# Kernel optimization log

Measured on AMD Instinct MI355X. Metric: run time of the kernel, lower is better.

The kernel has to match this reference:

```python
import jax, jax.numpy as jnp
import numpy as np

H = 4      # num_heads (== num_v_heads)
DK = 128   # head_k_dim
DV = 256   # head_v_dim = head_dim * expand_v
NH = 2     # num_householder
HID = 1024 # hidden_size
KSZ = 4    # conv_size
EPS = 1e-5 # norm_eps


def short_conv(x, w):
    """Causal depthwise conv1d + SiLU. x: [B,T,C], w: [C,K]."""
    K = w.shape[1]
    T = x.shape[1]
    xp = jnp.pad(x, ((0, 0), (K - 1, 0), (0, 0)))
    y = sum(xp[:, i:i + T, :] * w[:, i] for i in range(K))
    return jax.nn.silu(y)


def l2norm(x, eps=1e-6):
    return x * jax.lax.rsqrt(jnp.sum(x * x, axis=-1, keepdims=True) + eps)


def setup_inputs() -> dict:
    key = jax.random.key(0)
    ks = jax.random.split(key, 16)
    s = 0.02
    B, T = 2, 1024
    return {
        "hidden_states": jax.random.normal(ks[0], (B, T, HID), jnp.float32),
        "Wq": jax.random.normal(ks[1], (HID, H * DK), jnp.float32) * s,
        "Wk": jax.random.normal(ks[2], (HID, NH * H * DK), jnp.float32) * s,
        "Wv": jax.random.normal(ks[3], (HID, NH * H * DV), jnp.float32) * s,
        "Wb": jax.random.normal(ks[4], (HID, NH * H), jnp.float32) * s,
        "Wa": jax.random.normal(ks[5], (HID, H), jnp.float32) * s,
        "Wg": jax.random.normal(ks[6], (HID, H * DV), jnp.float32) * s,
        "Wo": jax.random.normal(ks[7], (H * DV, HID), jnp.float32) * s,
        "A_log": jnp.log(jax.random.uniform(ks[8], (H,), jnp.float32, 0.5, 8.0)),
        "dt_bias": jax.random.normal(ks[9], (H,), jnp.float32) * 0.1,
        "wq_conv": jax.random.normal(ks[10], (H * DK, KSZ), jnp.float32) * 0.2,
        "wk_conv": jax.random.normal(ks[11], (NH * H * DK, KSZ), jnp.float32) * 0.2,
        "wv_conv": jax.random.normal(ks[12], (NH * H * DV, KSZ), jnp.float32) * 0.2,
        "o_norm_weight": jnp.ones((DV,), jnp.float32),
    }


def reference(hidden_states, Wq, Wk, Wv, Wb, Wa, Wg, Wo, A_log, dt_bias,
              wq_conv, wk_conv, wv_conv, o_norm_weight):
    B, T, _ = hidden_states.shape
    # projections + short conv (+ SiLU)
    q = short_conv(hidden_states @ Wq, wq_conv).reshape(B, T, H, DK)
    k = short_conv(hidden_states @ Wk, wk_conv).reshape(B, T, NH, H, DK)
    v = short_conv(hidden_states @ Wv, wv_conv).reshape(B, T, NH, H, DV)
    q = l2norm(q)
    k = l2norm(k)
    # beta: sigmoid * 2 (allow_neg_eigval), layout '(n h)'
    beta = 2.0 * jax.nn.sigmoid(hidden_states @ Wb).reshape(B, T, NH, H)
    # forget gate per token/head
    g = -jnp.exp(A_log) * jax.nn.softplus(hidden_states @ Wa + dt_bias)  # [B,T,H]

    def step(S, x):
        # S: [B,H,DK,DV]
        q_t, k_t, v_t, b_t, g_t = x
        S = S * jnp.exp(g_t)[..., None, None]  # token-level decay
        for i in range(NH):  # sequential Householder delta updates
            ki, vi, bi = k_t[:, i], v_t[:, i], b_t[:, i]
            kv = jnp.einsum('bhk,bhkv->bhv', ki, S)
            S = S + bi[..., None, None] * jnp.einsum('bhk,bhv->bhkv', ki, vi - kv)
        o_t = jnp.einsum('bhk,bhkv->bhv', q_t, S)
        return S, o_t

    xs = (q.transpose(1, 0, 2, 3), k.transpose(1, 0, 2, 3, 4),
          v.transpose(1, 0, 2, 3, 4), beta.transpose(1, 0, 2, 3),
          g.transpose(1, 0, 2))
    S0 = jnp.zeros((B, H, DK, DV), hidden_states.dtype)
    _, o = jax.lax.scan(jax.checkpoint(step), S0, xs)
    o = o.transpose(1, 0, 2, 3)  # [B,T,H,DV]

    # gated RMSNorm (FusedRMSNormGated): rmsnorm(o)*w * silu(gate)
    gate = (hidden_states @ Wg).reshape(B, T, H, DV)
    o = o * jax.lax.rsqrt(jnp.mean(o * o, axis=-1, keepdims=True) + EPS) * o_norm_weight
    o = o * jax.nn.silu(gate)
    return o.reshape(B, T, H * DV) @ Wo
```

## Files before the change

### kernel.cpp

```cpp
#include <hip/hip_runtime.h>
#include <cstdint>
#include <cstddef>

#define H 4
#define DK 128
#define DV 256
#define NH 2
#define HID 1024
#define KSZ 4
#define NTOT 4608

typedef __bf16 bfx8 __attribute__((ext_vector_type(8)));
typedef float f32x4 __attribute__((ext_vector_type(4)));

__device__ __forceinline__ float wave_sum(float x) {
#pragma unroll
  for (int off = 1; off < 64; off <<= 1) x += __shfl_xor(x, off, 64);
  return x;
}

__device__ __forceinline__ ushort f2bf(float x) {
  uint u = __float_as_uint(x);
  return (ushort)((u + 0x7fffu + ((u >> 16) & 1u)) >> 16);
}

#define DPP_ADD(x, ctrl) \
  x += __int_as_float(__builtin_amdgcn_update_dpp(0, __float_as_int(x), ctrl, 0xf, 0xf, true))

template <int N>
__device__ __forceinline__ void dpp_reduce(float (&d)[N]) {
#pragma unroll
  for (int i = 0; i < N; i++) DPP_ADD(d[i], 0x111);
#pragma unroll
  for (int i = 0; i < N; i++) DPP_ADD(d[i], 0x112);
#pragma unroll
  for (int i = 0; i < N; i++) DPP_ADD(d[i], 0x114);
#pragma unroll
  for (int i = 0; i < N; i++) DPP_ADD(d[i], 0x118);
#pragma unroll
  for (int i = 0; i < N; i++) DPP_ADD(d[i], 0x142);
#pragma unroll
  for (int i = 0; i < N; i++) DPP_ADD(d[i], 0x143);
#pragma unroll
  for (int i = 0; i < N; i++)
    d[i] = __int_as_float(__builtin_amdgcn_readlane(__float_as_int(d[i]), 63));
}

__global__ __launch_bounds__(256) void cast_hs(const float* __restrict__ src,
                                               ushort* __restrict__ dst) {
  int i = blockIdx.x * 256 + threadIdx.x;
  float4 v = ((const float4*)src)[i];
  ushort4 o = {f2bf(v.x), f2bf(v.y), f2bf(v.z), f2bf(v.w)};
  ((ushort4*)dst)[i] = o;
}

__global__ __launch_bounds__(256) void tr_pack(const float* __restrict__ Wq,
                                               const float* __restrict__ Wk,
                                               const float* __restrict__ Wv,
                                               const float* __restrict__ Wg,
                                               ushort* __restrict__ Bt) {
  __shared__ float tile[32][33];
  int n0 = blockIdx.x * 32, k0 = blockIdx.y * 32;
  const float* src;
  int ld, nb;
  if (n0 < 512)       { src = Wq; ld = 512;  nb = n0; }
  else if (n0 < 1536) { src = Wk; ld = 1024; nb = n0 - 512; }
  else if (n0 < 3584) { src = Wv; ld = 2048; nb = n0 - 1536; }
  else                { src = Wg; ld = 1024; nb = n0 - 3584; }
  int tx = threadIdx.x & 31, ty = threadIdx.x >> 5;
#pragma unroll
  for (int i = 0; i < 4; i++)
    tile[ty + i * 8][tx] = src[(size_t)(k0 + ty + i * 8) * ld + nb + tx];
  __syncthreads();
#pragma unroll
  for (int i = 0; i < 4; i++)
    Bt[(size_t)(n0 + ty + i * 8) * 1024 + k0 + tx] = f2bf(tile[tx][ty + i * 8]);
}

__global__ __launch_bounds__(256) void tr_one(const float* __restrict__ W,
                                              ushort* __restrict__ Bt, int N) {
  __shared__ float tile[32][33];
  int n0 = blockIdx.x * 32, k0 = blockIdx.y * 32;
  int tx = threadIdx.x & 31, ty = threadIdx.x >> 5;
#pragma unroll
  for (int i = 0; i < 4; i++)
    tile[ty + i * 8][tx] = W[(size_t)(k0 + ty + i * 8) * N + n0 + tx];
  __syncthreads();
#pragma unroll
  for (int i = 0; i < 4; i++)
    Bt[(size_t)(n0 + ty + i * 8) * 1024 + k0 + tx] = f2bf(tile[tx][ty + i * 8]);
}

#define LDP 40
__global__ __launch_bounds__(256) void gemm_bf16(const ushort* __restrict__ A,
                                                 const ushort* __restrict__ Bt,
                                                 float* __restrict__ C,
                                                 int K, int ldc) {
  __shared__ __align__(16) ushort As[128][LDP];
  __shared__ __align__(16) ushort Bs[128][LDP];
  const int tid = threadIdx.x;
  const int lane = tid & 63, wave = tid >> 6;
  const int wr = wave >> 1, wc = wave & 1;
  const int row0 = blockIdx.y * 128, col0 = blockIdx.x * 128;
  const int r = tid >> 1, hf = tid & 1;

  f32x4 acc[4][4];
#pragma unroll
  for (int i = 0; i < 4; i++)
#pragma unroll
    for (int j = 0; j < 4; j++) acc[i][j] = {0.f, 0.f, 0.f, 0.f};

  const int lrow = lane & 15, lk = (lane >> 4) * 8;

  for (int k0 = 0; k0 < K; k0 += 32) {
    const float4* pa = (const float4*)(A + (size_t)(row0 + r) * K + k0 + hf * 16);
    const float4* pb = (const float4*)(Bt + (size_t)(col0 + r) * K + k0 + hf * 16);
    float4 a0 = pa[0], a1 = pa[1];
    float4 b0 = pb[0], b1 = pb[1];
    __syncthreads();
    *(float4*)&As[r][hf * 16] = a0;
    *(float4*)&As[r][hf * 16 + 8] = a1;
    *(float4*)&Bs[r][hf * 16] = b0;
    *(float4*)&Bs[r][hf * 16 + 8] = b1;
    __syncthreads();
    bfx8 af[4], bf[4];
#pragma unroll
    for (int mf = 0; mf < 4; mf++)
      af[mf] = *(const bfx8*)&As[wr * 64 + mf * 16 + lrow][lk];
#pragma unroll
    for (int nf = 0; nf < 4; nf++)
      bf[nf] = *(const bfx8*)&Bs[wc * 64 + nf * 16 + lrow][lk];
#pragma unroll
    for (int mf = 0; mf < 4; mf++)
#pragma unroll
      for (int nf = 0; nf < 4; nf++)
        acc[mf][nf] = __builtin_amdgcn_mfma_f32_16x16x32_bf16(af[mf], bf[nf], acc[mf][nf], 0, 0, 0);
  }
  const int crow = (lane >> 4) * 4, ccol = lane & 15;
#pragma unroll
  for (int mf = 0; mf < 4; mf++)
#pragma unroll
    for (int nf = 0; nf < 4; nf++)
#pragma unroll
      for (int rr = 0; rr < 4; rr++)
        C[(size_t)(row0 + wr * 64 + mf * 16 + crow + rr) * ldc + col0 + wc * 64 + nf * 16 + ccol] =
            acc[mf][nf][rr];
}

__global__ __launch_bounds__(256) void proj_bg(const float* __restrict__ hs,
                                               const float* __restrict__ Wb,
                                               const float* __restrict__ Wa,
                                               const float* __restrict__ A_log,
                                               const float* __restrict__ dt_bias,
                                               float* __restrict__ beta,
                                               float* __restrict__ g) {
  int row = blockIdx.x;
  int lane = threadIdx.x & 63;
  int wave = threadIdx.x >> 6;
  const float* x = hs + (size_t)row * HID;
  for (int out = wave; out < 12; out += 4) {
    float sum = 0.f;
    if (out < 8) {
      for (int k = lane; k < HID; k += 64) sum = fmaf(x[k], Wb[(size_t)k * 8 + out], sum);
    } else {
      int c = out - 8;
      for (int k = lane; k < HID; k += 64) sum = fmaf(x[k], Wa[(size_t)k * 4 + c], sum);
    }
    sum = wave_sum(sum);
    if (lane == 0) {
      if (out < 8) {
        beta[(size_t)row * 8 + out] = 2.f / (1.f + expf(-sum));
      } else {
        int h = out - 8;
        float xx = sum + dt_bias[h];
        float sp = (xx > 20.f) ? xx : log1pf(expf(xx));
        g[(size_t)row * 4 + h] = expf(-expf(A_log[h]) * sp);
      }
    }
  }
}

__global__ __launch_bounds__(128) void conv_q(const float* __restrict__ x, int ldx,
                                              const float* __restrict__ w,
                                              float* __restrict__ y, int T) {
  int rb = blockIdx.x;
  int h = rb % 4;
  int bt = rb / 4;
  int t = bt % T;
  int b = bt / T;
  int d = threadIdx.x;
  int c = h * 128 + d;
  const float* wc = w + (size_t)c * KSZ;
  float acc = 0.f;
#pragma unroll
  for (int i = 0; i < KSZ; i++) {
    int tt = t - (KSZ - 1) + i;
    if (tt >= 0) acc = fmaf(x[(size_t)(b * T + tt) * ldx + c], wc[i], acc);
  }
  float val = acc / (1.f + expf(-acc));
  float ss = wave_sum(val * val);
  __shared__ float sred[2];
  if ((threadIdx.x & 63) == 0) sred[threadIdx.x >> 6] = ss;
  __syncthreads();
  val *= rsqrtf(sred[0] + sred[1] + 1e-6f);
  y[((size_t)(b * 512 + (t >> 1)) * 4 + h) * 256 + (d >> 1) * 4 + (d & 1) + (t & 1) * 2] = val;
}

__global__ __launch_bounds__(128) void conv_k(const float* __restrict__ x, int ldx,
                                              const float* __restrict__ w,
                                              float* __restrict__ y, int T) {
  int rb = blockIdx.x;
  int gi = rb % 8;
  int bt = rb / 8;
  int t = bt % T;
  int b = bt / T;
  int i = gi >> 2, h = gi & 3;
  int d = threadIdx.x;
  int c = i * 512 + h * 128 + d;
  const float* wc = w + (size_t)c * KSZ;
  float acc = 0.f;
#pragma unroll
  for (int kk = 0; kk < KSZ; kk++) {
    int tt = t - (KSZ - 1) + kk;
    if (tt >= 0) acc = fmaf(x[(size_t)(b * T + tt) * ldx + c], wc[kk], acc);
  }
  float val = acc / (1.f + expf(-acc));
  float ss = wave_sum(val * val);
  __shared__ float sred[2];
  if ((threadIdx.x & 63) == 0) sred[threadIdx.x >> 6] = ss;
  __syncthreads();
  val *= rsqrtf(sred[0] + sred[1] + 1e-6f);
  y[((size_t)(b * T + t) * 4 + h) * 256 + (d >> 1) * 4 + (d & 1) + i * 2] = val;
}

__global__ __launch_bounds__(256) void conv_v(const float* __restrict__ x, int ldx,
                                              const float* __restrict__ w,
                                              float* __restrict__ y, int T) {
  int rb = blockIdx.x;
  int gi = rb % 8;
  int bt = rb / 8;
  int t = bt % T;
  int b = bt / T;
  int i = gi >> 2, h = gi & 3;
  int d = threadIdx.x;
  int c = i * 1024 + h * 256 + d;
  const float* wc = w + (size_t)c * KSZ;
  float acc = 0.f;
#pragma unroll
  for (int kk = 0; kk < KSZ; kk++) {
    int tt = t - (KSZ - 1) + kk;
    if (tt >= 0) acc = fmaf(x[(size_t)(b * T + tt) * ldx + c], wc[kk], acc);
  }
  float val = acc / (1.f + expf(-acc));
  y[((size_t)(b * 512 + (t >> 1)) * 4 + h) * 1024 + d * 4 + (t & 1) * 2 + i] = val;
}

__global__ __launch_bounds__(256) void cross_dots2(const float* __restrict__ kbuf2,
                                                   const float* __restrict__ qbuf2,
                                                   const float* __restrict__ beta,
                                                   const float* __restrict__ gam,
                                                   float* __restrict__ rec) {
  int idx = blockIdx.x * 4 + (threadIdx.x >> 6);
  int lane = threadIdx.x & 63;
  int h = idx & 3, tp = (idx >> 2) & 511, b = idx >> 11;
  int t = 2 * tp;
  const float4 kA = *(const float4*)&kbuf2[((size_t)(b * 1024 + t) * 4 + h) * 256 + lane * 4];
  const float4 kB = *(const float4*)&kbuf2[((size_t)(b * 1024 + t + 1) * 4 + h) * 256 + lane * 4];
  const float4 qv = *(const float4*)&qbuf2[(size_t)idx * 256 + lane * 4];
  float d[12];
  d[0] = kA.z * kA.x + kA.w * kA.y;
  d[1] = kB.x * kA.x + kB.y * kA.y;
  d[2] = kB.x * kA.z + kB.y * kA.w;
  d[3] = kB.z * kA.x + kB.w * kA.y;
  d[4] = kB.z * kA.z + kB.w * kA.w;
  d[5] = kB.z * kB.x + kB.w * kB.y;
  d[6] = qv.x * kA.x + qv.y * kA.y;
  d[7] = qv.x * kA.z + qv.y * kA.w;
  d[8] = qv.z * kA.x + qv.w * kA.y;
  d[9] = qv.z * kA.z + qv.w * kA.w;
  d[10] = qv.z * kB.x + qv.w * kB.y;
  d[11] = qv.z * kB.z + qv.w * kB.w;
  dpp_reduce(d);
  int bt = b * 1024 + t;
  float b0 = beta[(size_t)(bt * 2 + 0) * 4 + h];
  float b1 = beta[(size_t)(bt * 2 + 1) * 4 + h];
  float b2 = beta[(size_t)(bt * 2 + 2) * 4 + h];
  float b3 = beta[(size_t)(bt * 2 + 3) * 4 + h];
  float gt = gam[(size_t)bt * 4 + h];
  float gt1 = gam[(size_t)(bt + 1) * 4 + h];
  if (lane == 0) {
    float G2 = gt * gt1;
    float4* rp = (float4*)&rec[(size_t)idx * 24];
    rp[0] = {b0 * gt, b1 * gt, b1 * d[0], gt};
    rp[1] = {b2 * G2, b2 * gt1 * d[1], b2 * gt1 * d[2], gt1};
    rp[2] = {b3 * G2, b3 * gt1 * d[3], b3 * gt1 * d[4], b3 * d[5]};
    rp[3] = {d[6], d[7], G2, b0};
    rp[4] = {gt1 * d[8], gt1 * d[9], d[10], d[11]};
    rp[5] = {b1, b2, b3, 0.f};
  }
}

__global__ __launch_bounds__(256, 2) void scan2(const float4* __restrict__ kb,
                                                const float4* __restrict__ qb,
                                                const float4* __restrict__ vb,
                                                const float4* __restrict__ rb,
                                                float* __restrict__ o) {
  const int lane = threadIdx.x & 63;
  const int wave = __builtin_amdgcn_readfirstlane(threadIdx.x >> 6);
  const int bh = blockIdx.x & 7;
  const int cb = blockIdx.x >> 3;
  const int b = bh >> 2, h = bh & 3;
  const int col = cb * 4 + wave;

  const float4* kp = kb + ((size_t)(b * 1024) * 4 + h) * 64 + lane + 128;
  const float4* qp = qb + ((size_t)(b * 512) * 4 + h) * 64 + lane;
  const float4* vp = vb + ((size_t)(b * 512) * 4 + h) * 256 + col;
  const float4* rp = rb + ((size_t)(b * 512) * 4 + h) * 6;
  float* op = o + (size_t)(b * 1024) * NTOT + h * 256 + col;

  float sx = 0.f, sy = 0.f;

  float4 AkA, AkB, Aqv, Avv, AR0, AR1, AR2, AR3, AR4, AR5;
  float4 BkA, BkB, Bqv, Bvv, BR0, BR1, BR2, BR3, BR4, BR5;

#define LOADQ(P) { \
    P##kA = kp[-128]; \
    P##kB = kp[128]; \
    P##qv = qp[0]; \
    P##vv = vp[0]; \
    P##R0 = rp[0]; \
    P##R1 = rp[1]; \
    P##R2 = rp[2]; \
    P##R3 = rp[3]; \
    P##R4 = rp[4]; \
    P##R5 = rp[5]; \
    kp += 512; qp += 256; vp += 1024; rp += 24; }

#define STEPQ(P) { \
    float r[6]; \
    r[0] = P##kA.x * sx + P##kA.y * sy; \
    r[1] = P##kA.z * sx + P##kA.w * sy; \
    r[2] = P##kB.x * sx + P##kB.y * sy; \
    r[3] = P##kB.z * sx + P##kB.w * sy; \
    r[4] = P##qv.x * sx + P##qv.y * sy; \
    r[5] = P##qv.z * sx + P##qv.w * sy; \
    dpp_reduce(r); \
    float c0 = fmaf(-P##R0.x, r[0], P##R3.w * P##vv.x); \
    float c1 = fmaf(-P##R0.z, c0, fmaf(-P##R0.y, r[1], P##R5.x * P##vv.y)); \
    float c2 = fmaf(-P##R1.z, c1, fmaf(-P##R1.y, c0, fmaf(-P##R1.x, r[2], P##R5.y * P##vv.z))); \
    float c3 = fmaf(-P##R2.w, c2, fmaf(-P##R2.z, c1, fmaf(-P##R2.y, c0, \
               fmaf(-P##R2.x, r[3], P##R5.z * P##vv.w)))); \
    float ot = fmaf(P##R3.y, c1, fmaf(P##R3.x, c0, P##R0.w * r[4])); \
    float ot1 = fmaf(P##R4.w, c3, fmaf(P##R4.z, c2, fmaf(P##R4.y, c1, \
                fmaf(P##R4.x, c0, P##R3.z * r[5])))); \
    float g0 = P##R1.w * c0, g1 = P##R1.w * c1; \
    sx = fmaf(c3, P##kB.z, fmaf(c2, P##kB.x, fmaf(g1, P##kA.z, fmaf(g0, P##kA.x, P##R3.z * sx)))); \
    sy = fmaf(c3, P##kB.w, fmaf(c2, P##kB.y, fmaf(g1, P##kA.w, fmaf(g0, P##kA.y, P##R3.z * sy)))); \
    if (lane == 0) { op[0] = ot; op[NTOT] = ot1; } \
    op += 2 * NTOT; }

  LOADQ(A)
  LOADQ(B)
  for (int it = 0; it < 255; ++it) {
    STEPQ(A) LOADQ(A)
    STEPQ(B) LOADQ(B)
  }
  STEPQ(A)
  STEPQ(B)
#undef LOADQ
#undef STEPQ
}

__global__ __launch_bounds__(256) void post_norm_gate(const float* __restrict__ o,
                                                      const float* __restrict__ gate,
                                                      const float* __restrict__ w,
                                                      ushort* __restrict__ obf) {
  int rb = blockIdx.x;
  int bt = rb >> 2, h = rb & 3;
  int tid = threadIdx.x;
  size_t ob = (size_t)bt * NTOT + h * 256 + tid;
  float ov = o[ob];
  float ss = wave_sum(ov * ov);
  __shared__ float sred[4];
  if ((tid & 63) == 0) sred[tid >> 6] = ss;
  __syncthreads();
  float tot = sred[0] + sred[1] + sred[2] + sred[3];
  float rms = rsqrtf(tot * (1.f / 256.f) + 1e-5f);
  float gt = gate[(size_t)bt * NTOT + h * 256 + tid];
  float val = ov * rms * w[tid] * (gt / (1.f + expf(-gt)));
  obf[(size_t)bt * HID + h * 256 + tid] = f2bf(val);
}

extern "C" void kernel_launch(void* const* d_in, const int* in_sizes, int n_in,
                              void* d_out, int out_size, void* d_ws, size_t ws_size,
                              hipStream_t stream) {
  const float* hs      = (const float*)d_in[0];
  const float* Wq      = (const float*)d_in[1];
  const float* Wk      = (const float*)d_in[2];
  const float* Wv      = (const float*)d_in[3];
  const float* Wb      = (const float*)d_in[4];
  const float* Wa      = (const float*)d_in[5];
  const float* Wg      = (const float*)d_in[6];
  const float* Wo      = (const float*)d_in[7];
  const float* A_log   = (const float*)d_in[8];
  const float* dt_bias = (const float*)d_in[9];
  const float* wq_conv = (const float*)d_in[10];
  const float* wk_conv = (const float*)d_in[11];
  const float* wv_conv = (const float*)d_in[12];
  const float* o_w     = (const float*)d_in[13];
  float* out = (float*)d_out;

  const int B = 2, T = 1024, M = B * T;

  float* ws    = (float*)d_ws;
  float* qkvg  = ws;
  float* kbuf  = qkvg + (size_t)M * NTOT;
  float* vbuf  = kbuf + (size_t)M * 1024;
  float* betab = vbuf + (size_t)M * 2048;
  float* gb    = betab + (size_t)M * 8;
  float* recb  = gb + (size_t)M * 4;
  float* qbuf  = out;

  ushort* bqkvgT = (ushort*)kbuf;
  ushort* hsb    = (ushort*)(vbuf + (size_t)524288);
  ushort* woT = (ushort*)kbuf;
  ushort* obf = (ushort*)vbuf;

  cast_hs<<<(M * HID / 4) / 256, 256, 0, stream>>>(hs, hsb);
  tr_pack<<<dim3(NTOT / 32, HID / 32), 256, 0, stream>>>(Wq, Wk, Wv, Wg, bqkvgT);
  gemm_bf16<<<dim3(NTOT / 128, M / 128), 256, 0, stream>>>(hsb, bqkvgT, qkvg, HID, NTOT);
  proj_bg<<<M, 256, 0, stream>>>(hs, Wb, Wa, A_log, dt_bias, betab, gb);
  conv_q<<<M * 4, 128, 0, stream>>>(qkvg + 0, NTOT, wq_conv, qbuf, T);
  conv_k<<<M * 8, 128, 0, stream>>>(qkvg + 512, NTOT, wk_conv, kbuf, T);
  conv_v<<<M * 8, 256, 0, stream>>>(qkvg + 1536, NTOT, wv_conv, vbuf, T);
  cross_dots2<<<M * H / 8, 256, 0, stream>>>(kbuf, qbuf, betab, gb, recb);
  scan2<<<512, 256, 0, stream>>>((const float4*)kbuf, (const float4*)qbuf,
                                 (const float4*)vbuf, (const float4*)recb, qkvg);
  post_norm_gate<<<M * H, 256, 0, stream>>>(qkvg, qkvg + 3584, o_w, obf);
  tr_one<<<dim3(HID / 32, HID / 32), 256, 0, stream>>>(Wo, woT, HID);
  gemm_bf16<<<dim3(HID / 128, M / 128), 256, 0, stream>>>(obf, woT, out, HID, HID);
}
```

Measured before the change: 428.2 us.

## Split scan wave into two half-waves each owning one state column

The recurrent scan kernel now assigns one value column to each 32-lane half-wave instead of one per full wave. Each lane holds four state elements instead of two, and the cross-lane reduction stops at 32 lanes, finishing with a ds_swizzle broadcast rather than a readlane. The kernel is launched as 1024 single-wave blocks instead of 512 four-wave blocks. This halves the number of waves running the serial recurrence and shortens the reduction chain per step, but each lane carries more registers and loads, and there are fewer waves to hide latency.

```diff
diff --git a/kernel.cpp b/kernel.cpp
--- a/kernel.cpp
+++ b/kernel.cpp
@@ -44,6 +44,26 @@
 #pragma unroll
   for (int i = 0; i < N; i++)
     d[i] = __int_as_float(__builtin_amdgcn_readlane(__float_as_int(d[i]), 63));
+}
+
+__device__ __forceinline__ float swz31(float x) {
+  return __int_as_float(__builtin_amdgcn_ds_swizzle(__float_as_int(x), 0x3E0));
+}
+
+template <int N>
+__device__ __forceinline__ void dpp_reduce32(float (&d)[N]) {
+#pragma unroll
+  for (int i = 0; i < N; i++) DPP_ADD(d[i], 0x111);
+#pragma unroll
+  for (int i = 0; i < N; i++) DPP_ADD(d[i], 0x112);
+#pragma unroll
+  for (int i = 0; i < N; i++) DPP_ADD(d[i], 0x114);
+#pragma unroll
+  for (int i = 0; i < N; i++) DPP_ADD(d[i], 0x118);
+#pragma unroll
+  for (int i = 0; i < N; i++) DPP_ADD(d[i], 0x142);
+#pragma unroll
+  for (int i = 0; i < N; i++) d[i] = swz31(d[i]);
 }
 
 __global__ __launch_bounds__(256) void cast_hs(const float* __restrict__ src,
@@ -300,63 +320,61 @@
   }
 }
 
-__global__ __launch_bounds__(256, 2) void scan2(const float4* __restrict__ kb,
-                                                const float4* __restrict__ qb,
-                                                const float4* __restrict__ vb,
-                                                const float4* __restrict__ rb,
-                                                float* __restrict__ o) {
+__global__ __launch_bounds__(64, 1) void scan2(const float4* __restrict__ kb,
+                                               const float4* __restrict__ qb,
+                                               const float4* __restrict__ vb,
+                                               const float4* __restrict__ rb,
+                                               float* __restrict__ o) {
   const int lane = threadIdx.x & 63;
-  const int wave = __builtin_amdgcn_readfirstlane(threadIdx.x >> 6);
+  const int l32 = lane & 31;
   const int bh = blockIdx.x & 7;
-  const int cb = blockIdx.x >> 3;
+  const int cp = blockIdx.x >> 3;
   const int b = bh >> 2, h = bh & 3;
-  const int col = cb * 4 + wave;
-
-  const float4* kp = kb + ((size_t)(b * 1024) * 4 + h) * 64 + lane + 128;
-  const float4* qp = qb + ((size_t)(b * 512) * 4 + h) * 64 + lane;
+  const int col = cp * 2 + (lane >> 5);
+
+  const float4* kp = kb + ((size_t)(b * 1024) * 4 + h) * 64 + l32 * 2 + 128;
+  const float4* qp = qb + ((size_t)(b * 512) * 4 + h) * 64 + l32 * 2;
   const float4* vp = vb + ((size_t)(b * 512) * 4 + h) * 256 + col;
   const float4* rp = rb + ((size_t)(b * 512) * 4 + h) * 6;
   float* op = o + (size_t)(b * 1024) * NTOT + h * 256 + col;
 
-  float sx = 0.f, sy = 0.f;
-
-  float4 AkA, AkB, Aqv, Avv, AR0, AR1, AR2, AR3, AR4, AR5;
-  float4 BkA, BkB, Bqv, Bvv, BR0, BR1, BR2, BR3, BR4, BR5;
+  float s0 = 0.f, s1 = 0.f, s2 = 0.f, s3 = 0.f;
+
+  float4 AkA1, AkA2, AkB1, AkB2, Aqv1, Aqv2, Avv, AR0, AR1, AR2, AR3, AR4, AR5;
+  float4 BkA1, BkA2, BkB1, BkB2, Bqv1, Bqv2, Bvv, BR0, BR1, BR2, BR3, BR4, BR5;
 
 #define LOADQ(P) { \
-    P##kA = kp[-128]; \
-    P##kB = kp[128]; \
-    P##qv = qp[0]; \
-    P##vv = vp[0]; \
-    P##R0 = rp[0]; \
-    P##R1 = rp[1]; \
-    P##R2 = rp[2]; \
-    P##R3 = rp[3]; \
-    P##R4 = rp[4]; \
-    P##R5 = rp[5]; \
+    P##kA1 = kp[-128]; P##kA2 = kp[-127]; \
+    P##kB1 = kp[128];  P##kB2 = kp[129]; \
+    P##qv1 = qp[0];    P##qv2 = qp[1]; \
+    P##vv  = vp[0]; \
+    P##R0 = rp[0]; P##R1 = rp[1]; P##R2 = rp[2]; \
+    P##R3 = rp[3]; P##R4 = rp[4]; P##R5 = rp[5]; \
     kp += 512; qp += 256; vp += 1024; rp += 24; }
 
 #define STEPQ(P) { \
     float r[6]; \
-    r[0] = P##kA.x * sx + P##kA.y * sy; \
-    r[1] = P##kA.z * sx + P##kA.w * sy; \
-    r[2] = P##kB.x * sx + P##kB.y * sy; \
-    r[3] = P##kB.z * sx + P##kB.w * sy; \
-    r[4] = P##qv.x * sx + P##qv.y * sy; \
-    r[5] = P##qv.z * sx + P##qv.w * sy; \
-    dpp_reduce(r); \
+    r[0] = P##kA1.x * s0 + P##kA1.y * s1 + P##kA2.x * s2 + P##kA2.y * s3; \
+    r[1] = P##kA1.z * s0 + P##kA1.w * s1 + P##kA2.z * s2 + P##kA2.w * s3; \
+    r[2] = P##kB1.x * s0 + P##kB1.y * s1 + P##kB2.x * s2 + P##kB2.y * s3; \
+    r[3] = P##kB1.z * s0 + P##kB1.w * s1 + P##kB2.z * s2 + P##kB2.w * s3; \
+    r[4] = P##qv1.x * s0 + P##qv1.y * s1 + P##qv2.x * s2 + P##qv2.y * s3; \
+    r[5] = P##qv1.z * s0 + P##qv1.w * s1 + P##qv2.z * s2 + P##qv2.w * s3; \
+    dpp_reduce32(r); \
     float c0 = fmaf(-P##R0.x, r[0], P##R3.w * P##vv.x); \
     float c1 = fmaf(-P##R0.z, c0, fmaf(-P##R0.y, r[1], P##R5.x * P##vv.y)); \
     float c2 = fmaf(-P##R1.z, c1, fmaf(-P##R1.y, c0, fmaf(-P##R1.x, r[2], P##R5.y * P##vv.z))); \
     float c3 = fmaf(-P##R2.w, c2, fmaf(-P##R2.z, c1, fmaf(-P##R2.y, c0, \
                fmaf(-P##R2.x, r[3], P##R5.z * P##vv.w)))); \
-    float ot = fmaf(P##R3.y, c1, fmaf(P##R3.x, c0, P##R0.w * r[4])); \
+    float ot  = fmaf(P##R3.y, c1, fmaf(P##R3.x, c0, P##R0.w * r[4])); \
     float ot1 = fmaf(P##R4.w, c3, fmaf(P##R4.z, c2, fmaf(P##R4.y, c1, \
                 fmaf(P##R4.x, c0, P##R3.z * r[5])))); \
-    float g0 = P##R1.w * c0, g1 = P##R1.w * c1; \
-    sx = fmaf(c3, P##kB.z, fmaf(c2, P##kB.x, fmaf(g1, P##kA.z, fmaf(g0, P##kA.x, P##R3.z * sx)))); \
-    sy = fmaf(c3, P##kB.w, fmaf(c2, P##kB.y, fmaf(g1, P##kA.w, fmaf(g0, P##kA.y, P##R3.z * sy)))); \
-    if (lane == 0) { op[0] = ot; op[NTOT] = ot1; } \
+    float g0 = P##R1.w * c0, g1 = P##R1.w * c1, G2 = P##R3.z; \
+    s0 = fmaf(c3, P##kB1.z, fmaf(c2, P##kB1.x, fmaf(g1, P##kA1.z, fmaf(g0, P##kA1.x, G2 * s0)))); \
+    s1 = fmaf(c3, P##kB1.w, fmaf(c2, P##kB1.y, fmaf(g1, P##kA1.w, fmaf(g0, P##kA1.y, G2 * s1)))); \
+    s2 = fmaf(c3, P##kB2.z, fmaf(c2, P##kB2.x, fmaf(g1, P##kA2.z, fmaf(g0, P##kA2.x, G2 * s2)))); \
+    s3 = fmaf(c3, P##kB2.w, fmaf(c2, P##kB2.y, fmaf(g1, P##kA2.w, fmaf(g0, P##kA2.y, G2 * s3)))); \
+    if (l32 == 0) { op[0] = ot; op[NTOT] = ot1; } \
     op += 2 * NTOT; }
 
   LOADQ(A)
@@ -434,7 +452,7 @@
   conv_k<<<M * 8, 128, 0, stream>>>(qkvg + 512, NTOT, wk_conv, kbuf, T);
   conv_v<<<M * 8, 256, 0, stream>>>(qkvg + 1536, NTOT, wv_conv, vbuf, T);
   cross_dots2<<<M * H / 8, 256, 0, stream>>>(kbuf, qbuf, betab, gb, recb);
-  scan2<<<512, 256, 0, stream>>>((const float4*)kbuf, (const float4*)qbuf,
+  scan2<<<1024, 64, 0, stream>>>((const float4*)kbuf, (const float4*)qbuf,
                                  (const float4*)vbuf, (const float4*)recb, qkvg);
   post_norm_gate<<<M * H, 256, 0, stream>>>(qkvg, qkvg + 3584, o_w, obf);
   tr_one<<<dim3(HID / 32, HID / 32), 256, 0, stream>>>(Wo, woT, HID);
```

After: 495.5 us. 15.7% more time.
